# Kernel tuning notes

Hardware: AMD Instinct MI355X
Metric: run time of the kernel (lower is better)

## Reference

```python
import jax, jax.numpy as jnp
import numpy as np
from collections import deque

SIGMA_LOW = 0.02  # TreeFilter2D(sigma=0.02); high-level trees use sigma=1 (low_tree=False)


def bilinear_resize(x, oh, ow):
    # torch F.interpolate(mode='bilinear', align_corners=False)
    B, C, H, W = x.shape
    sy, sx = H / oh, W / ow
    ys = jnp.maximum((jnp.arange(oh, dtype=jnp.float32) + 0.5) * sy - 0.5, 0.0)
    xs = jnp.maximum((jnp.arange(ow, dtype=jnp.float32) + 0.5) * sx - 0.5, 0.0)
    y0 = jnp.clip(jnp.floor(ys).astype(jnp.int32), 0, H - 1)
    x0 = jnp.clip(jnp.floor(xs).astype(jnp.int32), 0, W - 1)
    y1 = jnp.minimum(y0 + 1, H - 1)
    x1 = jnp.minimum(x0 + 1, W - 1)
    wy = (ys - y0).reshape(oh, 1)
    wx = (xs - x0).reshape(1, ow)
    top, bot = x[:, :, y0, :], x[:, :, y1, :]
    v00, v01 = top[:, :, :, x0], top[:, :, :, x1]
    v10, v11 = bot[:, :, :, x0], bot[:, :, :, x1]
    return ((1 - wy) * (1 - wx)) * v00 + ((1 - wy) * wx) * v01 + (wy * (1 - wx)) * v10 + (wy * wx) * v11


def nearest_resize(x, oh, ow):
    B, C, H, W = x.shape
    yi = jnp.minimum((jnp.arange(oh) * (H / oh)).astype(jnp.int32), H - 1)
    xi = jnp.minimum((jnp.arange(ow) * (W / ow)).astype(jnp.int32), W - 1)
    return x[:, :, yi, :][:, :, :, xi]


def _mst_adj(feat, h, w):
    # Kruskal MST on 4-connected grid; edge weight = norm2_distance of features.
    n = h * w
    idx = np.arange(n).reshape(h, w)
    eu = np.concatenate([idx[:, :-1].ravel(), idx[:-1, :].ravel()])
    ev = np.concatenate([idx[:, 1:].ravel(), idx[1:, :].ravel()])
    f = feat.reshape(feat.shape[0], -1).astype(np.float64)
    d = ((f[:, eu] - f[:, ev]) ** 2).sum(axis=0)
    order = np.argsort(d, kind='stable')
    pa = np.arange(n)

    def find(a):
        r = a
        while pa[r] != r:
            r = pa[r]
        while pa[a] != r:
            pa[a], a = r, pa[a]
        return r

    adj = [[] for _ in range(n)]
    cnt = 0
    for e in order:
        u, v = int(eu[e]), int(ev[e])
        ru, rv = find(u), find(v)
        if ru != rv:
            pa[ru] = rv
            adj[u].append(v)
            adj[v].append(u)
            cnt += 1
            if cnt == n - 1:
                break
    return adj


def build_forest(embed):
    # embed: np [B,C,h,w] -> global parent array (ids b*n+i) + per-BFS-level node lists
    B, C, h, w = embed.shape
    n = h * w
    parent = np.arange(B * n)
    level = np.zeros(B * n, dtype=np.int64)
    for b in range(B):
        adj = _mst_adj(embed[b], h, w)
        lv = np.full(n, -1, dtype=np.int64)
        lv[0] = 0
        q = deque([0])
        while q:
            u = q.popleft()
            for v in adj[u]:
                if lv[v] < 0:
                    lv[v] = lv[u] + 1
                    parent[b * n + v] = b * n + u
                    q.append(v)
        level[b * n:(b + 1) * n] = lv
    d = int(level.max())
    levels = [np.nonzero(level == l)[0] for l in range(1, d + 1)]
    return jnp.asarray(parent), levels


def tree_filter(feature, embed, parent, levels, sigma):
    # feature [B,C,n], embed [B,Ce,n]; normalized tree filtering:
    # y_i = sum_j prod(path-edge-weights) x_j / sum_j prod(path-edge-weights)
    B, C, n = feature.shape
    ones = jnp.ones((B, 1, n), feature.dtype)
    xg = jnp.moveaxis(jnp.concatenate([feature, ones], axis=1), 0, 1).reshape(C + 1, B * n)
    eg = jnp.moveaxis(embed, 0, 1).reshape(embed.shape[1], B * n)
    wgt = jnp.exp(-((eg - eg[:, parent]) ** 2).sum(axis=0) / sigma)  # [B*n]; root entries unused
    # upward (leaf->root) subtree aggregation
    A = xg
    for idx in reversed(levels):
        A = A.at[:, parent[idx]].add(wgt[idx] * A[:, idx])
    # downward (root->leaf) completion
    F = A
    for idx in levels:
        F = F.at[:, idx].set(A[:, idx] + wgt[idx] * (F[:, parent[idx]] - wgt[idx] * A[:, idx]))
    y = F[:C] / F[C]
    return jnp.moveaxis(y.reshape(C, B, n), 0, 1)  # [B,C,n]


def setup_inputs() -> dict:
    key = jax.random.key(0)
    ks = jax.random.split(key, 6)
    B, K, h, w = 8, 4, 48, 48
    C = 512
    preds = jax.random.normal(ks[0], (B, K, h, w), jnp.float32)
    low_feats = jax.random.uniform(ks[1], (B, 3, 192, 192), jnp.float32) * 0.1
    hf1 = jax.random.normal(ks[2], (B, C, 24, 24), jnp.float32) * 0.05
    hf2 = jax.random.normal(ks[3], (B, C, 12, 12), jnp.float32) * 0.05
    hf3 = jax.random.normal(ks[4], (B, C, 6, 6), jnp.float32) * 0.05
    rois = (jax.random.uniform(ks[5], (B, 192, 192)) > 0.5).astype(jnp.float32)
    weight = jnp.asarray(0.4, jnp.float32)
    return {"preds": preds, "low_feats": low_feats, "high_feats_1": hf1,
            "high_feats_2": hf2, "high_feats_3": hf3, "unlabeled_ROIs": rois,
            "weight": weight}


def reference(preds, low_feats, high_feats_1, high_feats_2, high_feats_3, unlabeled_ROIs, weight):
    B, K, h, w = preds.shape
    low = bilinear_resize(low_feats, h, w)                     # no_grad in original
    roi = nearest_resize(unlabeled_ROIs[:, None], h, w)        # [B,1,h,w]
    N = roi.sum()
    prob = jax.nn.softmax(preds, axis=1)
    probf = prob.reshape(B, K, -1)
    roif = roi.reshape(B, 1, -1)

    parent0, lv0 = build_forest(np.asarray(low))
    AS = tree_filter(probf, low.reshape(B, low.shape[1], -1), parent0, lv0, SIGMA_LOW)

    loss = jnp.zeros((), preds.dtype)
    for hf in (high_feats_1, high_feats_2, high_feats_3):
        hfi = bilinear_resize(hf, h, w)
        p, lv = build_forest(np.asarray(hfi))
        AS_k = tree_filter(AS, hfi.reshape(B, hfi.shape[1], -1), p, lv, 1.0)
        loss = loss + (roif * jnp.abs(probf - AS_k)).sum()
    loss = jnp.where(N > 0, loss / N, loss)
    return weight * loss
```

## Files before the change

kernel.cpp:

```cpp
#include <hip/hip_runtime.h>
#include <math.h>


#define HH 48
#define WW 48
#define NN (HH*WW)
#define EHH (HH*(WW-1))
#define EEE (2*EHH)
#define BB 8
#define KK 4
#define TPB 256
#define TPE 512
#define TPW 1024
#define TPF 512
#define NPL 5
#define NPN 5
#define LVE (2*(NN-1))
#define RIPT ((LVE+TPW-1)/TPW)
#define NIPT ((NN+TPW-1)/TPW)
#define SENTN 0xFFFFu
#define MAXT 12

#define SSTRIDE_W (4*NN+8)
#define PK_OFF 0
#define D_OFF (4*NN)

__device__ __forceinline__ void edge_uv(int e,int& u,int& v){
  if(e<EHH){ int r=e/(WW-1); int c=e-r*(WW-1); u=r*WW+c; v=u+1; }
  else     { int t=e-EHH; u=t; v=t+WW; }
}

__device__ __forceinline__ void pick_src(int f, const float* lowf, const float* hf1,
                                         const float* hf2, const float* hf3,
                                         const float*& src, int& sh, int& C){
  if(f==0){src=lowf; sh=192; C=3;}
  else if(f==1){src=hf1; sh=24; C=512;}
  else if(f==2){src=hf2; sh=12; C=512;}
  else        {src=hf3; sh=6;  C=512;}
}

__global__ __launch_bounds__(TPE) void k_edges(
  const float* __restrict__ lowf, const float* __restrict__ hf1,
  const float* __restrict__ hf2, const float* __restrict__ hf3,
  const float* __restrict__ preds, float* __restrict__ probf,
  double* __restrict__ pd_low, double* __restrict__ pd_hf, int nchunk)
{
  __shared__ float up[4*NN+64];
  __shared__ int   y0t[48], y1t[48];
  __shared__ float wyt[48];
  const int tid=threadIdx.x;
  const int nEB=8+24*nchunk;

  if(blockIdx.x>=nEB){
    int t=(blockIdx.x-nEB)*TPE+tid;
    if(t<BB*NN){
      int b=t/NN, i=t-b*NN;
      const float* p=preds+(size_t)b*KK*NN+i;
      float x0=p[0],x1=p[NN],x2=p[2*NN],x3=p[3*NN];
      float mx=fmaxf(fmaxf(x0,x1),fmaxf(x2,x3));
      float e0=expf(x0-mx),e1=expf(x1-mx),e2=expf(x2-mx),e3=expf(x3-mx);
      float s=((e0+e1)+(e2+e3));
      float* q=probf+(size_t)b*KK*NN+i;
      q[0]=e0/s; q[NN]=e1/s; q[2*NN]=e2/s; q[3*NN]=e3/s;
    }
    return;
  }

  int pidx, chunk, hfidx=0;
  if(blockIdx.x<8){ pidx=blockIdx.x; chunk=0; }
  else { int t=blockIdx.x-8; hfidx=t/nchunk; chunk=t-hfidx*nchunk; pidx=8+hfidx; }
  const int f=pidx>>3, b=pidx&7;
  const float* src; int sh,C;
  pick_src(f,lowf,hf1,hf2,hf3,src,sh,C);
  const int shw=sh*sh;
  const float* srcb=src+(size_t)b*C*shw;
  const int cpc=(f==0)?3:(512/nchunk);
  const int c_begin=chunk*cpc;
  const int c_end=(c_begin+cpc<C)?(c_begin+cpc):C;

  if(tid<48){
    float sy=(float)sh/48.0f;
    float ys=fmaxf(((float)tid+0.5f)*sy-0.5f,0.0f);
    int y0=(int)ys; if(y0>sh-1) y0=sh-1;
    int y1=y0+1; if(y1>sh-1) y1=sh-1;
    y0t[tid]=y0; y1t[tid]=y1; wyt[tid]=ys-(float)y0;
  }

  double accH[NPN], accV[NPN];
  #pragma unroll
  for(int j=0;j<NPN;j++){ accH[j]=0.0; accV[j]=0.0; }

  for(int c0=c_begin;c0<c_end;c0+=4){
    const int nc=(c_end-c0<4)?(c_end-c0):4;
    __syncthreads();
    for(int i=tid;i<NN;i+=TPE){
      int r=i/WW, c=i-r*WW;
      int y0=y0t[r], y1=y1t[r]; float wy=wyt[r];
      int x0=y0t[c], x1=y1t[c]; float wx=wyt[c];
      float w00=(1.0f-wy)*(1.0f-wx), w01=(1.0f-wy)*wx;
      float w10=wy*(1.0f-wx),        w11=wy*wx;
      int o00=y0*sh+x0, o01=y0*sh+x1, o10=y1*sh+x0, o11=y1*sh+x1;
      const float* pl=srcb+(size_t)c0*shw;
      for(int cc=0;cc<nc;cc++){
        const float* p=pl+(size_t)cc*shw;
        up[cc*NN+i]=w00*p[o00]+w01*p[o01]+w10*p[o10]+w11*p[o11];
      }
    }
    __syncthreads();
    #pragma unroll
    for(int j=0;j<NPN;j++){
      int u=tid+j*TPE;
      if(u<NN){
        int r=u/WW, c=u-r*WW;
        bool hOK=(c<WW-1), vOK=(r<HH-1);
        for(int cc=0;cc<nc;cc++){
          const float* pu=up+cc*NN+u;
          float a=pu[0], b1=pu[1], c1=pu[WW];
          if(hOK){ double d=(double)a-(double)b1; accH[j]=fma(d,d,accH[j]); }
          if(vOK){ double d=(double)a-(double)c1; accV[j]=fma(d,d,accV[j]); }
        }
      }
    }
  }
  double* outp=(f==0)? pd_low+(size_t)pidx*EEE
                     : pd_hf+((size_t)hfidx*nchunk+chunk)*EEE;
  #pragma unroll
  for(int j=0;j<NPN;j++){
    int u=tid+j*TPE;
    if(u<NN){
      int r=u/WW, c=u-r*WW;
      if(c<WW-1) outp[r*(WW-1)+c]=accH[j];
      if(r<HH-1) outp[EHH+u]=accV[j];
    }
  }
}

__global__ __launch_bounds__(TPB) void k_redux(
  const double* __restrict__ pd_low, const double* __restrict__ pd_hf,
  int nchunk, double* __restrict__ dkeyG, int* __restrict__ cnt)
{
  int t=blockIdx.x*TPB+threadIdx.x;
  if(t==0) *cnt=0;
  if(t>=32*EEE) return;
  int pidx=t/EEE, e=t-pidx*EEE;
  double s;
  if(pidx<8) s=pd_low[(size_t)pidx*EEE+e];
  else {
    const double* p0=pd_hf+((size_t)(pidx-8)*nchunk)*EEE+e;
    s=0.0;
    for(int k=0;k<nchunk;k++) s+=p0[(size_t)k*EEE];
  }
  dkeyG[t]=s;
}

__global__ __launch_bounds__(TPW) void k_struct(
  const double* __restrict__ dkeyG, int* __restrict__ sbase,
  int2* __restrict__ apT)
{
  __shared__ __align__(16) char smem[123600];
  unsigned long long* keyE =(unsigned long long*)(smem+0);
  unsigned char*      mstf =(unsigned char*)(smem+36096);
  unsigned long long* best =(unsigned long long*)(smem+40608);
  int*                comp =(int*)(smem+59040);
  unsigned short*     uEdg =(unsigned short*)(smem+68256);
  int*                lnk  =(int*)(smem+77472);
  float4*             adjw =(float4*)(smem+40608);
  unsigned char*      adjS =(unsigned char*)(smem+77472);
  int*                chunkS=(int*)(smem+79776);
  unsigned int*       eA   =(unsigned int*)(smem+0);
  unsigned int*       eB   =(unsigned int*)(smem+18432);
  unsigned short*     uDE  =(unsigned short*)(smem+83872);
  int*                nodeoff=(int*)(smem+93088);
  int*                flags=(int*)(smem+123552);
  int*                ancA =(int*)(smem+0);
  float*              prmA =(float*)(smem+9216);
  int*                ancB =(int*)(smem+18432);
  float*              prmB =(float*)(smem+27648);

  const int tid=threadIdx.x;
  const int pidx=blockIdx.x;
  const int f=pidx>>3;
  const float sigma=(f==0)?0.02f:1.0f;
  const double* p0=dkeyG+(size_t)pidx*EEE;
  const int lane=tid&63, wid=tid>>6;

  {
    for(int e=tid;e<EEE;e+=TPW){
      int u,v; edge_uv(e,u,v);
      uEdg[e]=(unsigned short)u;
      keyE[e]=(((unsigned long long)__double_as_longlong(p0[e]))&~0x1FFFull)
              |(unsigned long long)e;
      mstf[e]=0;
    }
    for(int i=tid;i<NN;i+=TPW){ comp[i]=i; best[i]=~0ull; lnk[i]=i; }
    if(tid==0) flags[1]=0;
    __syncthreads();

    for(int round=0;round<20;++round){
      for(int i=tid;i<NN;i+=TPW) lnk[i]=i;
      for(int e=tid;e<EEE;e+=TPW){
        int u=uEdg[e]; int v=(e<EHH)?u+1:u+WW;
        int cu=comp[u], cv=comp[v];
        if(cu!=cv){
          unsigned long long k=keyE[e];
          atomicMin(&best[cu],k);
          atomicMin(&best[cv],k);
        }
      }
      __syncthreads();
      for(int i=tid;i<NN;i+=TPW){
        if(comp[i]==i && best[i]!=~0ull){
          int e=(int)(best[i]&0x1FFFull);
          int u=uEdg[e]; int v=(e<EHH)?u+1:u+WW;
          int cu=comp[u], cv=comp[v];
          int other=(cu==i)?cv:cu;
          bool mutual=((best[other]&0x1FFFull)==(unsigned long long)e);
          if(!mutual || other<i){ lnk[i]=other; mstf[e]=1; flags[1]=1; }
        }
      }
      __syncthreads();
      if(flags[1]==0) break;
      {
        volatile int* vl=lnk;
        for(int i=tid;i<NN;i+=TPW){
          int x=comp[i];
          int p=vl[x];
          int gp=vl[p];
          while(p!=gp){
            vl[x]=gp;
            x=p; p=gp; gp=vl[p];
          }
          comp[i]=p;
        }
      }
      for(int i=tid;i<NN;i+=TPW) best[i]=~0ull;
      if(tid==0) flags[1]=0;
      __syncthreads();
    }
    __syncthreads();

    for(int i=tid;i<NN;i+=TPW){
      int r=i/WW, c=i-r*WW;
      int mask=0; float4 w; w.x=0.0f; w.y=0.0f; w.z=0.0f; w.w=0.0f;
      if(c>0    && mstf[r*(WW-1)+c-1]){ mask|=1; w.x=expf(-(float)p0[r*(WW-1)+c-1]/sigma); }
      if(c<WW-1 && mstf[r*(WW-1)+c])  { mask|=2; w.y=expf(-(float)p0[r*(WW-1)+c]/sigma); }
      if(r>0    && mstf[EHH+i-WW])    { mask|=4; w.z=expf(-(float)p0[EHH+i-WW]/sigma); }
      if(r<HH-1 && mstf[EHH+i])       { mask|=8; w.w=expf(-(float)p0[EHH+i]/sigma); }
      adjw[i]=w;
      adjS[i]=(unsigned char)mask;
    }
    if(tid==0) flags[2]=0;
    __syncthreads();
  }

  {
    {
      const int base=tid*NIPT;
      int dg[NIPT], incl[NIPT]; int lsum=0;
      #pragma unroll
      for(int j=0;j<NIPT;j++){
        int i=base+j;
        dg[j]=(i<NN)?__popc((int)adjS[i]):0;
        lsum+=dg[j]; incl[j]=lsum;
      }
      int x=lsum;
      #pragma unroll
      for(int off=1;off<64;off<<=1){
        int y=__shfl_up(x,off,64);
        if(lane>=off) x+=y;
      }
      if(lane==63) chunkS[wid]=x;
      __syncthreads();
      if(wid==0 && lane<16){
        int w=chunkS[lane];
        #pragma unroll
        for(int off=1;off<16;off<<=1){
          int y=__shfl_up(w,off,64);
          if(lane>=off) w+=y;
        }
        chunkS[lane]=w;
      }
      __syncthreads();
      const int waveoff=(wid>0)?chunkS[wid-1]:0;
      const int myoff=x+waveoff-lsum;
      #pragma unroll
      for(int j=0;j<NIPT;j++){
        int i=base+j;
        if(i<NN) nodeoff[i]=myoff+incl[j]-dg[j];
      }
    }
    __syncthreads();

    for(int u=tid;u<NN;u+=TPW){
      int mu=adjS[u];
      int off=nodeoff[u];
      int m=mu;
      while(m){
        int d=__ffs(m)-1; m&=m-1;
        int ce=off+__popc(mu&((1<<d)-1));
        int v=(d==0)?u-1:(d==1)?u+1:(d==2)?u-WW:u+WW;
        int rd=d^1;
        int mv=adjS[v];
        int nd=rd;
        #pragma unroll
        for(int k2=4;k2>=1;k2--){ int dd=(rd+k2)&3; if(mv&(1<<dd)) nd=dd; }
        int ne=nodeoff[v]+__popc(mv&((1<<nd)-1));
        unsigned int nxt=(ne==0)?SENTN:(unsigned int)ne;
        uDE[ce]=(unsigned short)((u<<2)|d);
        eA[ce]=(nxt<<16)|1u;
      }
    }
    __syncthreads();

    unsigned int* P=eA; unsigned int* Q=eB;
    for(int r2=0;r2<13;r2++){
      for(int t=tid;t<LVE;t+=TPW){
        unsigned int pk=P[t];
        unsigned int dist=pk&0xFFFFu, nxt=pk>>16;
        if(nxt!=SENTN){
          unsigned int pk2=P[nxt];
          dist+=pk2&0xFFFFu;
          nxt=pk2>>16;
          pk=(nxt<<16)|dist;
        }
        Q[t]=pk;
      }
      __syncthreads();
      unsigned int* tmp=P; P=Q; Q=tmp;
    }
    for(int t=tid;t<LVE;t+=TPW){
      unsigned int dist=P[t]&0xFFFFu;
      Q[t]=(unsigned int)(LVE-(int)dist);
    }
    __syncthreads();

    int* scanA=(int*)P;
    for(int t=tid;t<LVE;t+=TPW){
      unsigned int pos=Q[t];
      int ud=uDE[t]; int u=ud>>2, d=ud&3;
      int v=(d==0)?u-1:(d==1)?u+1:(d==2)?u-WW:u+WW;
      int rce=nodeoff[v]+__popc(adjS[v]&((1<<(d^1))-1));
      unsigned int rpos=Q[rce];
      scanA[pos]=(pos<rpos)?1:-1;
    }
    __syncthreads();

    const int base=tid*RIPT;
    int vals[RIPT]; int lsum=0;
    #pragma unroll
    for(int j=0;j<RIPT;j++){
      int p=base+j;
      int v=(p<LVE)?scanA[p]:0;
      lsum+=v; vals[j]=lsum;
    }
    int x=lsum;
    #pragma unroll
    for(int off=1;off<64;off<<=1){
      int y=__shfl_up(x,off,64);
      if(lane>=off) x+=y;
    }
    if(lane==63) chunkS[wid]=x;
    __syncthreads();
    if(wid==0 && lane<16){
      int w=chunkS[lane];
      #pragma unroll
      for(int off=1;off<16;off<<=1){
        int y=__shfl_up(w,off,64);
        if(lane>=off) w+=y;
      }
      chunkS[lane]=w;
    }
    __syncthreads();
    const int waveoff=(wid>0)?chunkS[wid-1]:0;
    const int myoff=x+waveoff-lsum;
    int mymax=0;
    #pragma unroll
    for(int j=0;j<RIPT;j++){
      int p=base+j;
      if(p<LVE){ int s=vals[j]+myoff; scanA[p]=s; if(s>mymax) mymax=s; }
    }
    if(mymax>0) atomicMax(&flags[2],mymax);
    __syncthreads();

    int* sp=sbase+(size_t)pidx*SSTRIDE_W;
    int4* g_pk=(int4*)(sp+PK_OFF);
    if(tid==0){
      g_pk[0]=make_int4(0,__float_as_int(0.0f),0,0);
      sp[D_OFF]=flags[2];
    }
    for(int t=tid;t<LVE;t+=TPW){
      unsigned int pos=Q[t];
      int ud=uDE[t]; int u=ud>>2, d=ud&3;
      int v=(d==0)?u-1:(d==1)?u+1:(d==2)?u-WW:u+WW;
      int rce=nodeoff[v]+__popc(adjS[v]&((1<<(d^1))-1));
      unsigned int rpos=Q[rce];
      if(pos<rpos){
        float4 w4=adjw[u];
        float w=(d==0)?w4.x:(d==1)?w4.y:(d==2)?w4.z:w4.w;
        g_pk[v]=make_int4(u,__float_as_int(w),scanA[pos],0);
      }
    }
    __syncthreads();
  }

  {
    const int* sp=sbase+(size_t)pidx*SSTRIDE_W;
    const int4* g_pk=(const int4*)(sp+PK_OFF);
    const int maxD=flags[2];
    int T=1; while((1<<T)<=maxD) T++;
    int2* gAP=apT+(size_t)pidx*MAXT*NN;
    int* aP=ancA; int* aQ=ancB; float* pP=prmA; float* pQ=prmB;
    for(int i=tid;i<NN;i+=TPW){
      int4 rec=g_pk[i];
      aP[i]=rec.x; pP[i]=__int_as_float(rec.y);
      gAP[i]=make_int2(rec.x,rec.y);
    }
    __syncthreads();
    for(int t=1;t<T;t++){
      for(int i=tid;i<NN;i+=TPW){
        int a=aP[i];
        int a2=aP[a]; float pr=pP[i]*pP[a];
        aQ[i]=a2; pQ[i]=pr;
        gAP[(size_t)t*NN+i]=make_int2(a2,__float_as_int(pr));
      }
      __syncthreads();
      { int* t1=aP; aP=aQ; aQ=t1; float* t2=pP; pP=pQ; pQ=t2; }
    }
  }
}

__global__ __launch_bounds__(TPF) void k_fchan(
  const float* __restrict__ X, float* __restrict__ Fout,
  const int* __restrict__ sbase, const int2* __restrict__ apT,
  int pidx0, int dv)
{
  __shared__ float S[NN];
  __shared__ float Sb[NN];
  const int tid=threadIdx.x;
  const int pg=blockIdx.x/5, c=blockIdx.x%5;
  const int pidx=pidx0+pg;
  const int xb=pg&7;
  const int* sp=sbase+(size_t)pidx*SSTRIDE_W;
  const int4* g_pk=(const int4*)(sp+PK_OFF);
  const int maxD=sp[D_OFF];
  int T=1; while((1<<T)<=maxD) T++;
  const int2* apP=apT+(size_t)pidx*MAXT*NN;

  int dep[NPL]; float wv[NPL];
  #pragma unroll
  for(int j=0;j<NPL;j++){
    int i=tid+j*TPF;
    if(i<NN){
      int4 rec=g_pk[i];
      dep[j]=rec.z; wv[j]=__int_as_float(rec.y);
      float val=1.0f;
      if(c<4){
        if(dv){
          float inv=1.0f/X[((size_t)xb*5+4)*NN+i];
          val=X[((size_t)xb*5+c)*NN+i]*inv;
        } else {
          val=X[((size_t)xb*KK+c)*NN+i];
        }
      }
      S[i]=val;
    } else { dep[j]=-1; wv[j]=0.0f; }
  }
  __syncthreads();

  for(int t=0;t<T;t++){
    float sn[NPL]; int aj[NPL]; float pj[NPL];
    #pragma unroll
    for(int j=0;j<NPL;j++){
      int i=tid+j*TPF;
      if(i<NN){
        int2 ap=apP[(size_t)t*NN+i];
        sn[j]=S[i]; aj[j]=ap.x; pj[j]=__int_as_float(ap.y);
      }
      else { sn[j]=0.0f; aj[j]=0; pj[j]=0.0f; }
    }
    __syncthreads();
    int bit=1<<t;
    #pragma unroll
    for(int j=0;j<NPL;j++){
      if(dep[j]>=bit) atomicAdd(&S[aj[j]], pj[j]*sn[j]);
    }
    __syncthreads();
  }

  #pragma unroll
  for(int j=0;j<NPL;j++){
    int i=tid+j*TPF;
    if(i<NN){ float fq=1.0f-wv[j]*wv[j]; Sb[i]=fq*S[i]; }
  }
  __syncthreads();

  float* Sp=Sb; float* Sq=S;
  for(int t=0;t<T;t++){
    float bn[NPL];
    #pragma unroll
    for(int j=0;j<NPL;j++){
      int i=tid+j*TPF;
      if(i<NN){
        int2 ap=apP[(size_t)t*NN+i];
        bn[j]=fmaf(__int_as_float(ap.y),Sp[ap.x],Sp[i]);
      } else bn[j]=0.0f;
    }
    __syncthreads();
    #pragma unroll
    for(int j=0;j<NPL;j++){
      int i=tid+j*TPF;
      if(i<NN) Sq[i]=bn[j];
    }
    __syncthreads();
    { float* tmp=Sp; Sp=Sq; Sq=tmp; }
  }
  float* o=Fout+(size_t)blockIdx.x*NN;
  for(int i=tid;i<NN;i+=TPF) o[i]=Sp[i];
}

__global__ __launch_bounds__(TPB) void k_loss(
  const float* __restrict__ FB, const float* __restrict__ probf,
  const float* __restrict__ rois, float* __restrict__ partials,
  const float* __restrict__ wt, float* __restrict__ out, int* __restrict__ cnt)
{
  __shared__ float red[TPB];
  __shared__ int lastS;
  const int tid=threadIdx.x;
  const int fb=blockIdx.x;
  const int b=fb&7;
  const float* pb=probf+(size_t)b*KK*NN;
  float part=0.0f;
  for(int i=tid;i<NN;i+=TPB){
    int r=i/WW, c2=i-r*WW;
    float roi=rois[(size_t)b*(192*192)+(4*r)*192+(4*c2)];
    float inv=1.0f/FB[((size_t)fb*5+4)*NN+i];
    float s=fabsf(pb[i]      -FB[((size_t)fb*5+0)*NN+i]*inv)
          + fabsf(pb[NN+i]   -FB[((size_t)fb*5+1)*NN+i]*inv)
          + fabsf(pb[2*NN+i] -FB[((size_t)fb*5+2)*NN+i]*inv)
          + fabsf(pb[3*NN+i] -FB[((size_t)fb*5+3)*NN+i]*inv);
    part+=roi*s;
  }
  red[tid]=part; __syncthreads();
  for(int s2=TPB/2;s2>0;s2>>=1){ if(tid<s2) red[tid]+=red[tid+s2]; __syncthreads(); }
  if(tid==0){
    partials[fb]=red[0];
    __threadfence();
    int old=atomicAdd(cnt,1);
    lastS=(old==3*BB-1);
  }
  __syncthreads();
  if(!lastS) return;

  float n=0.0f;
  for(int t=tid;t<BB*NN;t+=TPB){
    int b2=t/NN, i=t-b2*NN; int r=i/WW, c=i-r*WW;
    n += rois[(size_t)b2*(192*192)+(4*r)*192+(4*c)];
  }
  red[tid]=n; __syncthreads();
  for(int s=TPB/2;s>0;s>>=1){ if(tid<s) red[tid]+=red[tid+s]; __syncthreads(); }
  if(tid==0){
    float loss=0.0f;
    for(int j=0;j<3*BB;j++) loss+=partials[j];
    float N=red[0];
    out[0]=wt[0]*((N>0.0f)?(loss/N):loss);
  }
}

extern "C" void kernel_launch(void* const* d_in, const int* in_sizes, int n_in,
                              void* d_out, int out_size, void* d_ws, size_t ws_size,
                              hipStream_t stream) {
  (void)in_sizes; (void)n_in; (void)out_size;
  const float* preds=(const float*)d_in[0];
  const float* lowf =(const float*)d_in[1];
  const float* hf1  =(const float*)d_in[2];
  const float* hf2  =(const float*)d_in[3];
  const float* hf3  =(const float*)d_in[4];
  const float* rois =(const float*)d_in[5];
  const float* wt   =(const float*)d_in[6];
  float* out=(float*)d_out;

  char* ws=(char*)d_ws;
  float* partials=(float*)ws;
  int*   cnt=(int*)(ws+128);
  float* probf=(float*)(ws+256);
  size_t sb_off=256+(size_t)2*BB*KK*NN*4;
  int*   sbase=(int*)(ws+sb_off);
  size_t dk_off=sb_off+(size_t)32*SSTRIDE_W*4;
  double* dkeyG=(double*)(ws+dk_off);
  size_t pl_off=dk_off+(size_t)32*EEE*8;
  double* pd_low=(double*)(ws+pl_off);
  size_t ph_off=pl_off+(size_t)8*EEE*8;
  double* pd_hf=(double*)(ws+ph_off);

  int2*  apT=(int2*)(ws+ph_off);
  float* FA =(float*)(ws+ph_off+(size_t)32*MAXT*NN*8);
  float* FB =(float*)(ws+ph_off+(size_t)32*MAXT*NN*8+(size_t)40*NN*4);

  int nchunk=32;
  if(ph_off+(size_t)24*32*EEE*8>ws_size) nchunk=16;

  const int nEB=8+24*nchunk;
  const int nSM=(BB*NN+TPE-1)/TPE;
  k_edges<<<nEB+nSM,TPE,0,stream>>>(lowf,hf1,hf2,hf3,preds,probf,pd_low,pd_hf,nchunk);
  k_redux<<<(32*EEE+TPB-1)/TPB,TPB,0,stream>>>(pd_low,pd_hf,nchunk,dkeyG,cnt);
  k_struct<<<32,TPW,0,stream>>>(dkeyG,sbase,apT);
  k_fchan<<<40,TPF,0,stream>>>(probf,FA,sbase,apT,0,0);
  k_fchan<<<120,TPF,0,stream>>>(FA,FB,sbase,apT,8,1);
  k_loss<<<3*BB,TPB,0,stream>>>(FB,probf,rois,partials,wt,out,cnt);
}
```

Before: 206.0 us.

## Drop Euler-tour depth scan; orient tree edges by distance and use zero-weight root padding

Removes the prefix-scan depth computation over the Euler tour. Tree edges are now oriented by comparing list-ranking distances directly. Node depth is no longer stored; the root's ancestor probability is zero, so pointer-jumping products vanish past the root. The number of jump levels is found by checking whether any product is nonzero, and the filter kernels do unconditional atomic adds. This cuts a scan and several block barriers in k_struct and the int4 record traffic, at the cost of always-executed atomics, including ones that add zero.

```diff
diff --git a/kernel.cpp b/kernel.cpp
--- a/kernel.cpp
+++ b/kernel.cpp
@@ -16,14 +16,9 @@
 #define NPL 5
 #define NPN 5
 #define LVE (2*(NN-1))
-#define RIPT ((LVE+TPW-1)/TPW)
 #define NIPT ((NN+TPW-1)/TPW)
 #define SENTN 0xFFFFu
 #define MAXT 12
-
-#define SSTRIDE_W (4*NN+8)
-#define PK_OFF 0
-#define D_OFF (4*NN)
 
 __device__ __forceinline__ void edge_uv(int e,int& u,int& v){
   if(e<EHH){ int r=e/(WW-1); int c=e-r*(WW-1); u=r*WW+c; v=u+1; }
@@ -154,7 +149,7 @@
 }
 
 __global__ __launch_bounds__(TPW) void k_struct(
-  const double* __restrict__ dkeyG, int* __restrict__ sbase,
+  const double* __restrict__ dkeyG, int* __restrict__ Tg,
   int2* __restrict__ apT)
 {
   __shared__ __align__(16) char smem[123600];
@@ -183,6 +178,7 @@
   const float sigma=(f==0)?0.02f:1.0f;
   const double* p0=dkeyG+(size_t)pidx*EEE;
   const int lane=tid&63, wid=tid>>6;
+  int2* apT0=apT+(size_t)pidx*MAXT*NN;
 
   {
     for(int e=tid;e<EEE;e+=TPW){
@@ -249,7 +245,6 @@
       adjw[i]=w;
       adjS[i]=(unsigned char)mask;
     }
-    if(tid==0) flags[2]=0;
     __syncthreads();
   }
 
@@ -328,110 +323,52 @@
       __syncthreads();
       unsigned int* tmp=P; P=Q; Q=tmp;
     }
+
+    if(tid==0) apT0[0]=make_int2(0,__float_as_int(0.0f));
     for(int t=tid;t<LVE;t+=TPW){
-      unsigned int dist=P[t]&0xFFFFu;
-      Q[t]=(unsigned int)(LVE-(int)dist);
-    }
-    __syncthreads();
-
-    int* scanA=(int*)P;
-    for(int t=tid;t<LVE;t+=TPW){
-      unsigned int pos=Q[t];
       int ud=uDE[t]; int u=ud>>2, d=ud&3;
       int v=(d==0)?u-1:(d==1)?u+1:(d==2)?u-WW:u+WW;
       int rce=nodeoff[v]+__popc(adjS[v]&((1<<(d^1))-1));
-      unsigned int rpos=Q[rce];
-      scanA[pos]=(pos<rpos)?1:-1;
-    }
-    __syncthreads();
-
-    const int base=tid*RIPT;
-    int vals[RIPT]; int lsum=0;
-    #pragma unroll
-    for(int j=0;j<RIPT;j++){
-      int p=base+j;
-      int v=(p<LVE)?scanA[p]:0;
-      lsum+=v; vals[j]=lsum;
-    }
-    int x=lsum;
-    #pragma unroll
-    for(int off=1;off<64;off<<=1){
-      int y=__shfl_up(x,off,64);
-      if(lane>=off) x+=y;
-    }
-    if(lane==63) chunkS[wid]=x;
-    __syncthreads();
-    if(wid==0 && lane<16){
-      int w=chunkS[lane];
-      #pragma unroll
-      for(int off=1;off<16;off<<=1){
-        int y=__shfl_up(w,off,64);
-        if(lane>=off) w+=y;
-      }
-      chunkS[lane]=w;
-    }
-    __syncthreads();
-    const int waveoff=(wid>0)?chunkS[wid-1]:0;
-    const int myoff=x+waveoff-lsum;
-    int mymax=0;
-    #pragma unroll
-    for(int j=0;j<RIPT;j++){
-      int p=base+j;
-      if(p<LVE){ int s=vals[j]+myoff; scanA[p]=s; if(s>mymax) mymax=s; }
-    }
-    if(mymax>0) atomicMax(&flags[2],mymax);
-    __syncthreads();
-
-    int* sp=sbase+(size_t)pidx*SSTRIDE_W;
-    int4* g_pk=(int4*)(sp+PK_OFF);
-    if(tid==0){
-      g_pk[0]=make_int4(0,__float_as_int(0.0f),0,0);
-      sp[D_OFF]=flags[2];
-    }
-    for(int t=tid;t<LVE;t+=TPW){
-      unsigned int pos=Q[t];
-      int ud=uDE[t]; int u=ud>>2, d=ud&3;
-      int v=(d==0)?u-1:(d==1)?u+1:(d==2)?u-WW:u+WW;
-      int rce=nodeoff[v]+__popc(adjS[v]&((1<<(d^1))-1));
-      unsigned int rpos=Q[rce];
-      if(pos<rpos){
+      unsigned int dist=P[t]&0xFFFFu, rdist=P[rce]&0xFFFFu;
+      if(dist>rdist){
         float4 w4=adjw[u];
         float w=(d==0)?w4.x:(d==1)?w4.y:(d==2)?w4.z:w4.w;
-        g_pk[v]=make_int4(u,__float_as_int(w),scanA[pos],0);
+        apT0[v]=make_int2(u,__float_as_int(w));
       }
     }
     __syncthreads();
   }
 
   {
-    const int* sp=sbase+(size_t)pidx*SSTRIDE_W;
-    const int4* g_pk=(const int4*)(sp+PK_OFF);
-    const int maxD=flags[2];
-    int T=1; while((1<<T)<=maxD) T++;
-    int2* gAP=apT+(size_t)pidx*MAXT*NN;
+    for(int t=tid;t<MAXT;t+=TPW) chunkS[t]=0;
     int* aP=ancA; int* aQ=ancB; float* pP=prmA; float* pQ=prmB;
     for(int i=tid;i<NN;i+=TPW){
-      int4 rec=g_pk[i];
+      int2 rec=apT0[i];
       aP[i]=rec.x; pP[i]=__int_as_float(rec.y);
-      gAP[i]=make_int2(rec.x,rec.y);
-    }
-    __syncthreads();
-    for(int t=1;t<T;t++){
+    }
+    __syncthreads();
+    int T=MAXT;
+    for(int t=1;t<MAXT;t++){
+      int any=0;
       for(int i=tid;i<NN;i+=TPW){
         int a=aP[i];
         int a2=aP[a]; float pr=pP[i]*pP[a];
         aQ[i]=a2; pQ[i]=pr;
-        gAP[(size_t)t*NN+i]=make_int2(a2,__float_as_int(pr));
-      }
-      __syncthreads();
+        apT0[(size_t)t*NN+i]=make_int2(a2,__float_as_int(pr));
+        if(pr!=0.0f) any=1;
+      }
+      if(any) chunkS[t]=1;
+      __syncthreads();
+      if(chunkS[t]==0){ T=t; break; }
       { int* t1=aP; aP=aQ; aQ=t1; float* t2=pP; pP=pQ; pQ=t2; }
     }
+    if(tid==0) Tg[pidx]=T;
   }
 }
 
 __global__ __launch_bounds__(TPF) void k_fchan(
   const float* __restrict__ X, float* __restrict__ Fout,
-  const int* __restrict__ sbase, const int2* __restrict__ apT,
+  const int* __restrict__ Tg, const int2* __restrict__ apT,
   int pidx0, int dv)
 {
   __shared__ float S[NN];
@@ -440,19 +377,16 @@
   const int pg=blockIdx.x/5, c=blockIdx.x%5;
   const int pidx=pidx0+pg;
   const int xb=pg&7;
-  const int* sp=sbase+(size_t)pidx*SSTRIDE_W;
-  const int4* g_pk=(const int4*)(sp+PK_OFF);
-  const int maxD=sp[D_OFF];
-  int T=1; while((1<<T)<=maxD) T++;
+  const int T=Tg[pidx];
   const int2* apP=apT+(size_t)pidx*MAXT*NN;
 
-  int dep[NPL]; float wv[NPL];
+  float wv[NPL];
   #pragma unroll
   for(int j=0;j<NPL;j++){
     int i=tid+j*TPF;
     if(i<NN){
-      int4 rec=g_pk[i];
-      dep[j]=rec.z; wv[j]=__int_as_float(rec.y);
+      int2 ap0=apP[i];
+      wv[j]=__int_as_float(ap0.y);
       float val=1.0f;
       if(c<4){
         if(dv){
@@ -463,7 +397,7 @@
         }
       }
       S[i]=val;
-    } else { dep[j]=-1; wv[j]=0.0f; }
+    } else wv[j]=0.0f;
   }
   __syncthreads();
 
@@ -479,10 +413,10 @@
       else { sn[j]=0.0f; aj[j]=0; pj[j]=0.0f; }
     }
     __syncthreads();
-    int bit=1<<t;
     #pragma unroll
     for(int j=0;j<NPL;j++){
-      if(dep[j]>=bit) atomicAdd(&S[aj[j]], pj[j]*sn[j]);
+      int i=tid+j*TPF;
+      if(i<NN) atomicAdd(&S[aj[j]], pj[j]*sn[j]);
     }
     __syncthreads();
   }
@@ -583,9 +517,9 @@
   float* partials=(float*)ws;
   int*   cnt=(int*)(ws+128);
   float* probf=(float*)(ws+256);
-  size_t sb_off=256+(size_t)2*BB*KK*NN*4;
-  int*   sbase=(int*)(ws+sb_off);
-  size_t dk_off=sb_off+(size_t)32*SSTRIDE_W*4;
+  size_t tg_off=256+(size_t)2*BB*KK*NN*4;
+  int*   Tg=(int*)(ws+tg_off);
+  size_t dk_off=tg_off+256;
   double* dkeyG=(double*)(ws+dk_off);
   size_t pl_off=dk_off+(size_t)32*EEE*8;
   double* pd_low=(double*)(ws+pl_off);
@@ -603,8 +537,8 @@
   const int nSM=(BB*NN+TPE-1)/TPE;
   k_edges<<<nEB+nSM,TPE,0,stream>>>(lowf,hf1,hf2,hf3,preds,probf,pd_low,pd_hf,nchunk);
   k_redux<<<(32*EEE+TPB-1)/TPB,TPB,0,stream>>>(pd_low,pd_hf,nchunk,dkeyG,cnt);
-  k_struct<<<32,TPW,0,stream>>>(dkeyG,sbase,apT);
-  k_fchan<<<40,TPF,0,stream>>>(probf,FA,sbase,apT,0,0);
-  k_fchan<<<120,TPF,0,stream>>>(FA,FB,sbase,apT,8,1);
+  k_struct<<<32,TPW,0,stream>>>(dkeyG,Tg,apT);
+  k_fchan<<<40,TPF,0,stream>>>(probf,FA,Tg,apT,0,0);
+  k_fchan<<<120,TPF,0,stream>>>(FA,FB,Tg,apT,8,1);
   k_loss<<<3*BB,TPB,0,stream>>>(FB,probf,rois,partials,wt,out,cnt);
 }
```

Result: slower. 210.5 us (+2.2%).
